# Kernel optimization log

Hardware: AMD Instinct MI355X
Metric: run time of the kernel (lower is better)

## Reference

```python
import jax, jax.numpy as jnp
import numpy as np

BASE_TEMP, MIN_TEMP, MAX_TEMP = 0.07, 0.04, 0.2
B, D = 4096, 768


def setup_inputs() -> dict:
    key = jax.random.key(0)
    k1, k2, k3 = jax.random.split(key, 3)
    return {
        "vision_features": jax.random.normal(k1, (B, D), dtype=jnp.float32),
        "text_features": jax.random.normal(k2, (B, D), dtype=jnp.float32),
        "match_ids": jax.random.randint(k3, (B,), 0, 1024, dtype=jnp.int64),
    }


def reference(vision_features, text_features, match_ids):
    # L2-normalize features along the feature dim
    v = vision_features / jnp.linalg.norm(vision_features, axis=1, keepdims=True)
    t = text_features / jnp.linalg.norm(text_features, axis=1, keepdims=True)
    sim = v @ t.T  # [B, B]

    n = match_ids.shape[0]
    match = match_ids[:, None] == match_ids[None, :]  # [B, B] bool, diag True
    mf = match.astype(sim.dtype)
    eye = jnp.eye(n, dtype=sim.dtype)
    pos_mask = mf * (1.0 - eye)          # diagonal zeroed
    neg_mask = 1.0 - mf                   # diagonal also zero (was match)

    pos_mean = (pos_mask * sim).sum() / jnp.maximum(1.0, pos_mask.sum())
    neg_mean = (neg_mask * sim).sum() / jnp.maximum(1.0, neg_mask.sum())
    separation = pos_mean - neg_mean
    temp = jnp.clip(BASE_TEMP * (0.8 + 0.4 * jnp.exp(-2.0 * separation)),
                    MIN_TEMP, MAX_TEMP)

    logits = sim / temp
    # v2t: for each row i, sum over positives j of (-logits[i,j] + lse(row i))
    lse_rows = jax.nn.logsumexp(logits, axis=1)  # [B]
    v2t = (mf * (lse_rows[:, None] - logits)).sum()
    # t2v: for each column i, sum over positives j of (-logits[j,i] + lse(col i))
    lse_cols = jax.nn.logsumexp(logits, axis=0)  # [B]
    t2v = (mf * (lse_cols[None, :] - logits)).sum()

    num_pos = mf.sum()  # includes diagonal, matching the torch code
    v2t = v2t / num_pos
    t2v = t2v / num_pos
    loss = (v2t + t2v) / 2.0
    return loss
```

## Files before the change

kernel.cpp:

```cpp
#include <hip/hip_runtime.h>
#include <hip/hip_bf16.h>

#define NB 4096
#define DD 768
#define NKT 12
#define NBLK 256

typedef float f32x4 __attribute__((ext_vector_type(4)));
typedef long i64x2 __attribute__((ext_vector_type(2)));
typedef unsigned int uint;

#define WAITVM(N) asm volatile("s_waitcnt vmcnt(" #N ")" ::: "memory")

__global__ void init_kernel(float* scal, uint* bars)
{
    int t = threadIdx.x;
    if (t < 16) scal[t] = 0.0f;
    bars[t] = 0u;
    bars[512 + t] = 0u;
}

__device__ __forceinline__ void grid_bar(uint* bars, uint phase, int rawb, int t)
{
    __syncthreads();
    if (t == 0) {
        int g = rawb & 15;
        uint prev = __hip_atomic_fetch_add(&bars[g * 16], 1u, __ATOMIC_ACQ_REL, __HIP_MEMORY_SCOPE_AGENT);
        if (prev == phase * 16u - 1u) {
            uint r = __hip_atomic_fetch_add(&bars[384], 1u, __ATOMIC_ACQ_REL, __HIP_MEMORY_SCOPE_AGENT);
            if (r == phase * 16u - 1u)
                __hip_atomic_store(&bars[448], phase, __ATOMIC_RELEASE, __HIP_MEMORY_SCOPE_AGENT);
        }
        while (__hip_atomic_load(&bars[448], __ATOMIC_RELAXED, __HIP_MEMORY_SCOPE_AGENT) < phase)
            __builtin_amdgcn_s_sleep(8);
        (void)__hip_atomic_load(&bars[448], __ATOMIC_ACQUIRE, __HIP_MEMORY_SCOPE_AGENT);
    }
    __syncthreads();
}

__device__ __forceinline__ void stage_range(
    unsigned char* ldsAll,
    const unsigned char* __restrict__ vhat8, const unsigned char* __restrict__ that8,
    int rowBase, int colBase, int T, int i0, int i1, int wid, int lane)
{
    int u = T & 3;
    const unsigned char* src = (wid >= 4) ? that8 : vhat8;
    int tb = (wid >= 4) ? colBase : rowBase;
    int w4 = wid & 3;
    int logc = (lane & 3) ^ ((lane >> 3) & 3);
    int rowIn = w4 * 64 + (lane >> 2);
    unsigned char* dbase = ldsAll + u * 32768 + ((wid >= 4) ? 16384 : 0) + w4 * 4096;
    #pragma unroll
    for (int i = i0; i <= i1; ++i) {
        const unsigned char* g = src + (size_t)(tb + rowIn + i * 16) * DD + T * 64 + logc * 16;
        __builtin_amdgcn_global_load_lds(
            (const __attribute__((address_space(1))) void*)g,
            (__attribute__((address_space(3))) void*)(dbase + i * 1024),
            16, 0, 0);
    }
}

__global__ __launch_bounds__(512, 2) void fused_kernel(
    const float* __restrict__ vf, const float* __restrict__ tf, const int* __restrict__ ids,
    unsigned char* __restrict__ vhat8, unsigned char* __restrict__ that8,
    float* scal, float* rs, float* cs, float* cntf, int* npart, uint* bars,
    float* __restrict__ out)
{
    __shared__ unsigned char ldsAll[4 * 32768];
    __shared__ int idr[256], idc[256];
    __shared__ float red[24];
    __shared__ float rs_l[256], cs_l[256];
    __shared__ int bp[16], wred_i[8];
    __shared__ float ra[8], rn[8];
    __shared__ float invT_sh, mf_sh;
    __shared__ uint tick_sh;

    int rawb = blockIdx.x;
    int t = threadIdx.x, wid = t >> 6, lane = t & 63;

    {
        f32x4 xr[4][3];
        uint* dsts[4];
        #pragma unroll
        for (int it = 0; it < 4; ++it) {
            int row = rawb * 32 + wid * 4 + it;
            const float* src;
            if (row < NB) { src = vf + (size_t)row * DD; dsts[it] = (uint*)(vhat8 + (size_t)row * DD); }
            else          { src = tf + (size_t)(row - NB) * DD; dsts[it] = (uint*)(that8 + (size_t)(row - NB) * DD); }
            xr[it][0] = __builtin_nontemporal_load((const f32x4*)(src + lane * 4));
            xr[it][1] = __builtin_nontemporal_load((const f32x4*)(src + 256 + lane * 4));
            xr[it][2] = __builtin_nontemporal_load((const f32x4*)(src + 512 + lane * 4));
        }
        int idreg[8];
        #pragma unroll
        for (int i = 0; i < 8; ++i) idreg[i] = ids[t + i * 512];

        #pragma unroll
        for (int it = 0; it < 4; ++it) {
            float s = 0.f;
            #pragma unroll
            for (int c = 0; c < 3; ++c)
                s += xr[it][c][0]*xr[it][c][0] + xr[it][c][1]*xr[it][c][1]
                   + xr[it][c][2]*xr[it][c][2] + xr[it][c][3]*xr[it][c][3];
            #pragma unroll
            for (int off = 1; off < 64; off <<= 1) s += __shfl_xor(s, off, 64);
            float scale = 1.0f / sqrtf(s);
            #pragma unroll
            for (int c = 0; c < 3; ++c) {
                int p = __builtin_amdgcn_cvt_pk_fp8_f32(xr[it][c][0] * scale, xr[it][c][1] * scale, 0, false);
                p = __builtin_amdgcn_cvt_pk_fp8_f32(xr[it][c][2] * scale, xr[it][c][3] * scale, p, true);
                dsts[it][c * 64 + lane] = (uint)p;
            }
        }
        int* idsh = (int*)ldsAll;
        #pragma unroll
        for (int i = 0; i < 8; ++i) idsh[t + i * 512] = idreg[i];
    }
    __syncthreads();
    if (t == 0)
        __hip_atomic_fetch_add(&bars[512 + (rawb >> 3) * 16], 1u, __ATOMIC_ACQ_REL, __HIP_MEMORY_SCOPE_AGENT);

    {
        int* idsh = (int*)ldsAll;
        int sub = t >> 5, l32 = t & 31;
        int my = idsh[rawb * 16 + sub];
        const int4* idsh4 = (const int4*)idsh;
        int c = 0;
        #pragma unroll 8
        for (int j = l32; j < NB / 4; j += 32) {
            int4 v = idsh4[j];
            c += (v.x == my) + (v.y == my) + (v.z == my) + (v.w == my);
        }
        #pragma unroll
        for (int off = 16; off > 0; off >>= 1) c += __shfl_down(c, off, 32);
        if (l32 == 0) { cntf[rawb * 16 + sub] = (float)c; bp[sub] = c; }
    }
    if (t < 32) rs[rawb * 32 + t] = 0.0f;
    __syncthreads();
    if (t == 0) {
        int s = 0;
        #pragma unroll
        for (int i = 0; i < 16; ++i) s += bp[i];
        npart[rawb] = s;
    }

    int rg = rawb & 7, sq = rawb >> 3;
    int by = (rg >> 1) * 4 + (sq >> 3);
    int bx = (rg & 1) * 8 + (sq & 7);
    int rowBase = by * 256, colBase = bx * 256;
    int wr = wid >> 2, wc = wid & 3;
    int fr = lane & 15, g = lane >> 4;

    __syncthreads();
    if (t == 0) {
        uint* fA = &bars[512 + by * 16];
        uint* fB = &bars[512 + (16 + bx) * 16];
        while (__hip_atomic_load(fA, __ATOMIC_RELAXED, __HIP_MEMORY_SCOPE_AGENT) < 8u)
            __builtin_amdgcn_s_sleep(4);
        while (__hip_atomic_load(fB, __ATOMIC_RELAXED, __HIP_MEMORY_SCOPE_AGENT) < 8u)
            __builtin_amdgcn_s_sleep(4);
        (void)__hip_atomic_load(fA, __ATOMIC_ACQUIRE, __HIP_MEMORY_SCOPE_AGENT);
        (void)__hip_atomic_load(fB, __ATOMIC_ACQUIRE, __HIP_MEMORY_SCOPE_AGENT);
    }
    __syncthreads();

    f32x4 acc[8][4];
    #pragma unroll
    for (int m = 0; m < 8; ++m)
        #pragma unroll
        for (int n = 0; n < 4; ++n) acc[m][n] = (f32x4){0.f, 0.f, 0.f, 0.f};

    int pcoff = (g ^ ((fr >> 1) & 3)) * 16;
    int aoffB = (wr * 128 + fr) * 64 + pcoff;
    int boffB = 16384 + (wc * 64 + fr) * 64 + pcoff;

    stage_range(ldsAll, vhat8, that8, rowBase, colBase, 0, 0, 3, wid, lane);
    stage_range(ldsAll, vhat8, that8, rowBase, colBase, 1, 0, 3, wid, lane);
    stage_range(ldsAll, vhat8, that8, rowBase, colBase, 2, 0, 3, wid, lane);
    WAITVM(8);
    __builtin_amdgcn_s_barrier();

    for (int T = 0; T < NKT; ++T) {
        const unsigned char* U = ldsAll + (T & 3) * 32768;
        i64x2 a0[4], bb[4];
        #pragma unroll
        for (int m = 0; m < 4; ++m) a0[m] = *(const i64x2*)(U + aoffB + m * 1024);
        #pragma unroll
        for (int n = 0; n < 4; ++n) bb[n] = *(const i64x2*)(U + boffB + n * 1024);
        if (T + 3 < NKT)
            stage_range(ldsAll, vhat8, that8, rowBase, colBase, T + 3, 0, 1, wid, lane);
        __builtin_amdgcn_s_barrier();
        __builtin_amdgcn_s_setprio(1);
        #pragma unroll
        for (int m = 0; m < 4; ++m)
            #pragma unroll
            for (int n = 0; n < 4; ++n) {
                acc[m][n] = __builtin_amdgcn_mfma_f32_16x16x32_fp8_fp8(a0[m][0], bb[n][0], acc[m][n], 0, 0, 0);
                acc[m][n] = __builtin_amdgcn_mfma_f32_16x16x32_fp8_fp8(a0[m][1], bb[n][1], acc[m][n], 0, 0, 0);
            }
        __builtin_amdgcn_s_setprio(0);
        __builtin_amdgcn_s_barrier();
        i64x2 a1[4];
        #pragma unroll
        for (int m = 0; m < 4; ++m) a1[m] = *(const i64x2*)(U + aoffB + (m + 4) * 1024);
        if (T + 3 < NKT)
            stage_range(ldsAll, vhat8, that8, rowBase, colBase, T + 3, 2, 3, wid, lane);
        __builtin_amdgcn_s_barrier();
        __builtin_amdgcn_s_setprio(1);
        #pragma unroll
        for (int m = 0; m < 4; ++m)
            #pragma unroll
            for (int n = 0; n < 4; ++n) {
                acc[m + 4][n] = __builtin_amdgcn_mfma_f32_16x16x32_fp8_fp8(a1[m][0], bb[n][0], acc[m + 4][n], 0, 0, 0);
                acc[m + 4][n] = __builtin_amdgcn_mfma_f32_16x16x32_fp8_fp8(a1[m][1], bb[n][1], acc[m + 4][n], 0, 0, 0);
            }
        __builtin_amdgcn_s_setprio(0);
        if (T < NKT - 3)       { WAITVM(8); }
        else if (T == NKT - 3) { WAITVM(4); }
        else if (T == NKT - 2) { WAITVM(0); }
        __builtin_amdgcn_s_barrier();
    }

    if (t < 256) idr[t] = ids[rowBase + t];
    else         idc[t - 256] = ids[colBase + (t - 256)];
    __syncthreads();
    {
        float tsum = 0.f, msum = 0.f, dsum = 0.f;
        #pragma unroll
        for (int m = 0; m < 8; ++m) {
            int rl = wr * 128 + m * 16 + g * 4;
            #pragma unroll
            for (int n = 0; n < 4; ++n) {
                int cl = wc * 64 + n * 16 + fr;
                int colId = idc[cl];
                int gj = colBase + cl;
                #pragma unroll
                for (int r = 0; r < 4; ++r) {
                    float val = acc[m][n][r];
                    tsum += val;
                    if (idr[rl + r] == colId) msum += val;
                    if (rowBase + rl + r == gj) dsum += val;
                }
            }
        }
        #pragma unroll
        for (int off = 32; off > 0; off >>= 1) {
            tsum += __shfl_down(tsum, off, 64);
            msum += __shfl_down(msum, off, 64);
            dsum += __shfl_down(dsum, off, 64);
        }
        if (lane == 0) { red[wid] = tsum; red[8 + wid] = msum; red[16 + wid] = dsum; }
        __syncthreads();
        if (t == 0) {
            float s0 = 0.f, s1 = 0.f, s2 = 0.f;
            #pragma unroll
            for (int w = 0; w < 8; ++w) { s0 += red[w]; s1 += red[8 + w]; s2 += red[16 + w]; }
            atomicAdd(&scal[0], s0);
            atomicAdd(&scal[1], s1);
            atomicAdd(&scal[2], s2);
        }
    }

    {
        int myn = (t < NBLK) ? npart[t] : 0;
        #pragma unroll
        for (int off = 32; off > 0; off >>= 1) myn += __shfl_down(myn, off, 64);
        if (lane == 0) wred_i[wid] = myn;
    }
    if (t < 256) { rs_l[t] = 0.0f; cs_l[t] = 0.0f; }

    grid_bar(bars, 1u, rawb, t);

    if (t == 0) {
        int npi = 0;
        #pragma unroll
        for (int w = 0; w < 8; ++w) npi += wred_i[w];
        float total = __hip_atomic_load(&scal[0], __ATOMIC_RELAXED, __HIP_MEMORY_SCOPE_AGENT);
        float mf    = __hip_atomic_load(&scal[1], __ATOMIC_RELAXED, __HIP_MEMORY_SCOPE_AGENT);
        float trace = __hip_atomic_load(&scal[2], __ATOMIC_RELAXED, __HIP_MEMORY_SCOPE_AGENT);
        float np = (float)npi;
        float pos_cnt = np - (float)NB;
        float neg_cnt = (float)NB * (float)NB - np;
        float pos_mean = (mf - trace) / fmaxf(1.0f, pos_cnt);
        float neg_mean = (total - mf) / fmaxf(1.0f, neg_cnt);
        float sep = pos_mean - neg_mean;
        float temp = 0.07f * (0.8f + 0.4f * expf(-2.0f * sep));
        temp = fminf(fmaxf(temp, 0.04f), 0.2f);
        invT_sh = 1.0f / temp;
        mf_sh = mf;
    }
    __syncthreads();
    float invT = invT_sh;

    #pragma unroll
    for (int m = 0; m < 8; ++m)
        #pragma unroll
        for (int n = 0; n < 4; ++n)
            #pragma unroll
            for (int r = 0; r < 4; ++r)
                acc[m][n][r] = __expf((acc[m][n][r] - 1.0f) * invT);
    #pragma unroll
    for (int m = 0; m < 8; ++m) {
        #pragma unroll
        for (int r = 0; r < 4; ++r) {
            float rp = 0.f;
            #pragma unroll
            for (int n = 0; n < 4; ++n) rp += acc[m][n][r];
            rp += __shfl_xor(rp, 1, 64);
            rp += __shfl_xor(rp, 2, 64);
            rp += __shfl_xor(rp, 4, 64);
            rp += __shfl_xor(rp, 8, 64);
            if (fr == 0) atomicAdd(&rs_l[wr * 128 + m * 16 + g * 4 + r], rp);
        }
    }
    #pragma unroll
    for (int n = 0; n < 4; ++n) {
        float cp = 0.f;
        #pragma unroll
        for (int m = 0; m < 8; ++m)
            #pragma unroll
            for (int r = 0; r < 4; ++r) cp += acc[m][n][r];
        cp += __shfl_xor(cp, 16, 64);
        cp += __shfl_xor(cp, 32, 64);
        if (g == 0) atomicAdd(&cs_l[wc * 64 + n * 16 + fr], cp);
    }
    __syncthreads();
    if (t < 256) {
        atomicAdd(&rs[rowBase + t], rs_l[t]);
        atomicAdd(&cs[colBase + t], cs_l[t]);
    }

    __syncthreads();
    if (t == 0) {
        uint prev = __hip_atomic_fetch_add(&bars[464], 1u, __ATOMIC_ACQ_REL, __HIP_MEMORY_SCOPE_AGENT);
        tick_sh = prev;
    }
    __syncthreads();
    if (tick_sh != NBLK - 1) return;

    {
        float a = 0.f, npl = 0.f;
        for (int i = t; i < NB; i += 512) {
            float cf = cntf[i];
            a += cf * (logf(rs[i]) + logf(cs[i]));
            npl += cf;
        }
        #pragma unroll
        for (int off = 32; off > 0; off >>= 1) {
            a += __shfl_down(a, off, 64);
            npl += __shfl_down(npl, off, 64);
        }
        if (lane == 0) { ra[wid] = a; rn[wid] = npl; }
        __syncthreads();
        if (t == 0) {
            float A = 0.f, np = 0.f;
            #pragma unroll
            for (int w = 0; w < 8; ++w) { A += ra[w]; np += rn[w]; }
            out[0] = (A + 2.0f * invT_sh * (np - mf_sh)) / (2.0f * np);
        }
    }
}

extern "C" void kernel_launch(void* const* d_in, const int* in_sizes, int n_in,
                              void* d_out, int out_size, void* d_ws, size_t ws_size,
                              hipStream_t stream)
{
    const float* vf  = (const float*)d_in[0];
    const float* tf  = (const float*)d_in[1];
    const int*   ids = (const int*)d_in[2];

    float* ws_f = (float*)d_ws;
    float* scal = ws_f;
    float* rs   = ws_f + 16;
    float* cs   = ws_f + 16 + 4096;
    float* cntf = ws_f + 16 + 8192;
    int* npart  = (int*)(ws_f + 16 + 12288);
    uint* bars  = (uint*)(ws_f + 16 + 12800);
    unsigned char* vhat8 = (unsigned char*)d_ws + 131072;
    unsigned char* that8 = vhat8 + (size_t)NB * DD;

    init_kernel<<<1, 512, 0, stream>>>(scal, bars);
    fused_kernel<<<NBLK, 512, 0, stream>>>(vf, tf, ids, vhat8, that8,
                                           scal, rs, cs, cntf, npart, bars, (float*)d_out);
}
```

Measured before the change: 77.44 us.

## Overlap match counting with GEMM prologue staging and atomically accumulate pair count

Moves the readiness spin-wait and the first three k-tile LDS stages ahead of the match-id counting, so the counting work overlaps with the asynchronous global-to-LDS loads. The id table moves to the fourth LDS buffer so it does not collide with the staged tiles. The per-block pair-count array and its post-GEMM reduction are replaced by a single global atomic counter in the scalar slot. Nontemporal loads of the input features also become plain loads. The prologue now depends on the other blocks' flags earlier, and the id table occupies buffer 3, which is safe only as long as buffer 3 is not staged before counting ends.

```diff
diff --git a/kernel.cpp b/kernel.cpp
--- a/kernel.cpp
+++ b/kernel.cpp
@@ -63,18 +63,19 @@
 __global__ __launch_bounds__(512, 2) void fused_kernel(
     const float* __restrict__ vf, const float* __restrict__ tf, const int* __restrict__ ids,
     unsigned char* __restrict__ vhat8, unsigned char* __restrict__ that8,
-    float* scal, float* rs, float* cs, float* cntf, int* npart, uint* bars,
+    float* scal, float* rs, float* cs, float* cntf, uint* bars,
     float* __restrict__ out)
 {
     __shared__ unsigned char ldsAll[4 * 32768];
     __shared__ int idr[256], idc[256];
     __shared__ float red[24];
     __shared__ float rs_l[256], cs_l[256];
-    __shared__ int bp[16], wred_i[8];
+    __shared__ int bp[16];
     __shared__ float ra[8], rn[8];
     __shared__ float invT_sh, mf_sh;
     __shared__ uint tick_sh;
 
+    int* np_acc = (int*)(scal + 3);
     int rawb = blockIdx.x;
     int t = threadIdx.x, wid = t >> 6, lane = t & 63;
 
@@ -87,9 +88,9 @@
             const float* src;
             if (row < NB) { src = vf + (size_t)row * DD; dsts[it] = (uint*)(vhat8 + (size_t)row * DD); }
             else          { src = tf + (size_t)(row - NB) * DD; dsts[it] = (uint*)(that8 + (size_t)(row - NB) * DD); }
-            xr[it][0] = __builtin_nontemporal_load((const f32x4*)(src + lane * 4));
-            xr[it][1] = __builtin_nontemporal_load((const f32x4*)(src + 256 + lane * 4));
-            xr[it][2] = __builtin_nontemporal_load((const f32x4*)(src + 512 + lane * 4));
+            xr[it][0] = *(const f32x4*)(src + lane * 4);
+            xr[it][1] = *(const f32x4*)(src + 256 + lane * 4);
+            xr[it][2] = *(const f32x4*)(src + 512 + lane * 4);
         }
         int idreg[8];
         #pragma unroll
@@ -112,7 +113,7 @@
                 dsts[it][c * 64 + lane] = (uint)p;
             }
         }
-        int* idsh = (int*)ldsAll;
+        int* idsh = (int*)(ldsAll + 3 * 32768);
         #pragma unroll
         for (int i = 0; i < 8; ++i) idsh[t + i * 512] = idreg[i];
     }
@@ -120,8 +121,31 @@
     if (t == 0)
         __hip_atomic_fetch_add(&bars[512 + (rawb >> 3) * 16], 1u, __ATOMIC_ACQ_REL, __HIP_MEMORY_SCOPE_AGENT);
 
+    int rg = rawb & 7, sq = rawb >> 3;
+    int by = (rg >> 1) * 4 + (sq >> 3);
+    int bx = (rg & 1) * 8 + (sq & 7);
+    int rowBase = by * 256, colBase = bx * 256;
+    int wr = wid >> 2, wc = wid & 3;
+    int fr = lane & 15, g = lane >> 4;
+
+    if (t == 0) {
+        uint* fA = &bars[512 + by * 16];
+        uint* fB = &bars[512 + (16 + bx) * 16];
+        while (__hip_atomic_load(fA, __ATOMIC_RELAXED, __HIP_MEMORY_SCOPE_AGENT) < 8u)
+            __builtin_amdgcn_s_sleep(4);
+        while (__hip_atomic_load(fB, __ATOMIC_RELAXED, __HIP_MEMORY_SCOPE_AGENT) < 8u)
+            __builtin_amdgcn_s_sleep(4);
+        (void)__hip_atomic_load(fA, __ATOMIC_ACQUIRE, __HIP_MEMORY_SCOPE_AGENT);
+        (void)__hip_atomic_load(fB, __ATOMIC_ACQUIRE, __HIP_MEMORY_SCOPE_AGENT);
+    }
+    __syncthreads();
+
+    stage_range(ldsAll, vhat8, that8, rowBase, colBase, 0, 0, 3, wid, lane);
+    stage_range(ldsAll, vhat8, that8, rowBase, colBase, 1, 0, 3, wid, lane);
+    stage_range(ldsAll, vhat8, that8, rowBase, colBase, 2, 0, 3, wid, lane);
+
     {
-        int* idsh = (int*)ldsAll;
+        int* idsh = (int*)(ldsAll + 3 * 32768);
         int sub = t >> 5, l32 = t & 31;
         int my = idsh[rawb * 16 + sub];
         const int4* idsh4 = (const int4*)idsh;
@@ -141,28 +165,10 @@
         int s = 0;
         #pragma unroll
         for (int i = 0; i < 16; ++i) s += bp[i];
-        npart[rawb] = s;
-    }
-
-    int rg = rawb & 7, sq = rawb >> 3;
-    int by = (rg >> 1) * 4 + (sq >> 3);
-    int bx = (rg & 1) * 8 + (sq & 7);
-    int rowBase = by * 256, colBase = bx * 256;
-    int wr = wid >> 2, wc = wid & 3;
-    int fr = lane & 15, g = lane >> 4;
-
-    __syncthreads();
-    if (t == 0) {
-        uint* fA = &bars[512 + by * 16];
-        uint* fB = &bars[512 + (16 + bx) * 16];
-        while (__hip_atomic_load(fA, __ATOMIC_RELAXED, __HIP_MEMORY_SCOPE_AGENT) < 8u)
-            __builtin_amdgcn_s_sleep(4);
-        while (__hip_atomic_load(fB, __ATOMIC_RELAXED, __HIP_MEMORY_SCOPE_AGENT) < 8u)
-            __builtin_amdgcn_s_sleep(4);
-        (void)__hip_atomic_load(fA, __ATOMIC_ACQUIRE, __HIP_MEMORY_SCOPE_AGENT);
-        (void)__hip_atomic_load(fB, __ATOMIC_ACQUIRE, __HIP_MEMORY_SCOPE_AGENT);
-    }
-    __syncthreads();
+        atomicAdd(np_acc, s);
+    }
+    WAITVM(8);
+    __builtin_amdgcn_s_barrier();
 
     f32x4 acc[8][4];
     #pragma unroll
@@ -173,12 +179,6 @@
     int pcoff = (g ^ ((fr >> 1) & 3)) * 16;
     int aoffB = (wr * 128 + fr) * 64 + pcoff;
     int boffB = 16384 + (wc * 64 + fr) * 64 + pcoff;
-
-    stage_range(ldsAll, vhat8, that8, rowBase, colBase, 0, 0, 3, wid, lane);
-    stage_range(ldsAll, vhat8, that8, rowBase, colBase, 1, 0, 3, wid, lane);
-    stage_range(ldsAll, vhat8, that8, rowBase, colBase, 2, 0, 3, wid, lane);
-    WAITVM(8);
-    __builtin_amdgcn_s_barrier();
 
     for (int T = 0; T < NKT; ++T) {
         const unsigned char* U = ldsAll + (T & 3) * 32768;
@@ -260,21 +260,12 @@
             atomicAdd(&scal[2], s2);
         }
     }
-
-    {
-        int myn = (t < NBLK) ? npart[t] : 0;
-        #pragma unroll
-        for (int off = 32; off > 0; off >>= 1) myn += __shfl_down(myn, off, 64);
-        if (lane == 0) wred_i[wid] = myn;
-    }
     if (t < 256) { rs_l[t] = 0.0f; cs_l[t] = 0.0f; }
 
     grid_bar(bars, 1u, rawb, t);
 
     if (t == 0) {
-        int npi = 0;
-        #pragma unroll
-        for (int w = 0; w < 8; ++w) npi += wred_i[w];
+        int npi = __hip_atomic_load(np_acc, __ATOMIC_RELAXED, __HIP_MEMORY_SCOPE_AGENT);
         float total = __hip_atomic_load(&scal[0], __ATOMIC_RELAXED, __HIP_MEMORY_SCOPE_AGENT);
         float mf    = __hip_atomic_load(&scal[1], __ATOMIC_RELAXED, __HIP_MEMORY_SCOPE_AGENT);
         float trace = __hip_atomic_load(&scal[2], __ATOMIC_RELAXED, __HIP_MEMORY_SCOPE_AGENT);
@@ -374,12 +365,11 @@
     float* rs   = ws_f + 16;
     float* cs   = ws_f + 16 + 4096;
     float* cntf = ws_f + 16 + 8192;
-    int* npart  = (int*)(ws_f + 16 + 12288);
     uint* bars  = (uint*)(ws_f + 16 + 12800);
     unsigned char* vhat8 = (unsigned char*)d_ws + 131072;
     unsigned char* that8 = vhat8 + (size_t)NB * DD;
 
     init_kernel<<<1, 512, 0, stream>>>(scal, bars);
     fused_kernel<<<NBLK, 512, 0, stream>>>(vf, tf, ids, vhat8, that8,
-                                           scal, rs, cs, cntf, npart, bars, (float*)d_out);
-}
+                                           scal, rs, cs, cntf, bars, (float*)d_out);
+}
```

Measured after the change: 76.13 us. About the same (-1.7%).
